# Optimization experiments

Hardware: AMD Instinct MI355X
Metric: run time of the kernel (lower is better)

Reference implementation:

```python
import jax, jax.numpy as jnp
import numpy as np

B, N, C = 2, 100000, 256
H, D, S = 8, 64, 64
INNER = H * D

def setup_inputs() -> dict:
    key = jax.random.key(0)
    ks = jax.random.split(key, 5)
    x = jax.random.normal(ks[0], (B, N, C), dtype=jnp.float32)
    W_x = jax.random.normal(ks[1], (C, INNER), dtype=jnp.float32) / np.sqrt(C)
    b_x = jnp.zeros((INNER,), dtype=jnp.float32)
    W_fx = jax.random.normal(ks[2], (C, INNER), dtype=jnp.float32) / np.sqrt(C)
    b_fx = jnp.zeros((INNER,), dtype=jnp.float32)
    W_slice = jax.random.normal(ks[3], (D, S), dtype=jnp.float32) / np.sqrt(D)
    b_slice = jnp.zeros((S,), dtype=jnp.float32)
    temperature = jnp.ones((1, 1, H, 1), dtype=jnp.float32) * 0.5
    return {"x": x, "W_x": W_x, "b_x": b_x, "W_fx": W_fx, "b_fx": b_fx,
            "W_slice": W_slice, "b_slice": b_slice, "temperature": temperature}

def reference(x, W_x, b_x, W_fx, b_fx, W_slice, b_slice, temperature):
    b, n, _ = x.shape
    # linear projections to (B, N, H, D)
    px = (x @ W_x + b_x).reshape(b, n, H, D)   # query-like projection
    fx = (x @ W_fx + b_fx).reshape(b, n, H, D) # feature (value) projection
    # slice logits (B, N, H, S)
    slice_proj = jnp.einsum('bnhd,ds->bnhs', px, W_slice) + b_slice
    temp = jnp.clip(temperature, 0.1, 5.0)     # (1,1,H,1), broadcast over S
    slice_weights = jax.nn.softmax(slice_proj / temp, axis=-1)  # (B,N,H,S)
    slice_norm = slice_weights.sum(axis=1)     # (B,H,S)
    # weighted aggregation of tokens into slice tokens (B,H,S,D)
    slice_token = jnp.einsum('bnhs,bnhd->bhsd', slice_weights, fx)
    slice_token = slice_token / (slice_norm[..., None] + 1e-5)
    return slice_token
```

## Files before the change

kernel.cpp:

```cpp
#include <hip/hip_runtime.h>
#include <hip/hip_bf16.h>
#include <cstdint>

#define B_     2
#define N_     100000
#define C_     256
#define H_     8
#define D_     64
#define S_     64
#define INNER_ 512

#define TILE_T 64
#define NTILES ((N_ + TILE_T - 1) / TILE_T)
#define PBLK   32

#define WEFFT_OFF 0
#define WFXT_OFF  262144
#define BIASE_OFF 524288
#define SLAB_OFF  526336
#define NSLAB_OFF (SLAB_OFF + B_*H_*PBLK*4096*4)
#define WS_BIG_END (NSLAB_OFF + B_*H_*PBLK*64*4)
#define ACC_OFF   526336
#define NRM_OFF   (ACC_OFF + B_*H_*S_*D_*4)
#define WS_SMALL_END (NRM_OFF + B_*H_*S_*4)

typedef __attribute__((ext_vector_type(8))) short short8;
typedef __attribute__((ext_vector_type(4))) float f32x4;

__device__ inline short f2bf(float f) {
    __hip_bfloat16 h = __float2bfloat16(f);
    short s; __builtin_memcpy(&s, &h, 2); return s;
}
__device__ inline uint32_t pk2(float a, float b) {
    __hip_bfloat162 h = __float22bfloat162_rn(float2{a, b});
    uint32_t u; __builtin_memcpy(&u, &h, 4); return u;
}

__global__ void prep_kernel(const float* __restrict__ W_x,
                            const float* __restrict__ b_x,
                            const float* __restrict__ W_fx,
                            const float* __restrict__ W_slice,
                            const float* __restrict__ b_slice,
                            const float* __restrict__ temperature,
                            uint8_t* __restrict__ wsb) {
    int wid  = (blockIdx.x * 256 + threadIdx.x) >> 6;
    int lane = threadIdx.x & 63;
    if (wid < H_ * C_) {
        int h = wid >> 8, k = wid & 255;
        float t = temperature[h]; t = fminf(fmaxf(t, 0.1f), 5.0f);
        float sc = 1.44269504088896f / t;
        const float* wx = W_x + k * INNER_ + h * 64;
        float a = 0.f;
        #pragma unroll 8
        for (int d = 0; d < D_; ++d)
            a = fmaf(wx[d], W_slice[d * 64 + lane], a);
        ((short*)(wsb + WEFFT_OFF))[(h * 64 + lane) * 256 + k] = f2bf(a * sc);
    } else if (wid < 2 * H_ * C_) {
        int j = wid - H_ * C_;
        int h = j >> 8, k = j & 255;
        ((short*)(wsb + WFXT_OFF))[(h * 64 + lane) * 256 + k] =
            f2bf(W_fx[k * INNER_ + h * 64 + lane]);
    } else if (wid < 2 * H_ * C_ + H_) {
        int h = wid - 2 * H_ * C_;
        float t = temperature[h]; t = fminf(fmaxf(t, 0.1f), 5.0f);
        float sc = 1.44269504088896f / t;
        float a = 0.f;
        #pragma unroll 8
        for (int d = 0; d < D_; ++d)
            a = fmaf(b_x[h * 64 + d], W_slice[d * 64 + lane], a);
        ((float*)(wsb + BIASE_OFF))[h * 64 + lane] = (a + b_slice[lane]) * sc;
    }
}

template<bool SLAB>
__global__ __launch_bounds__(512, 4) void main_kernel(
        const float* __restrict__ x,
        const float* __restrict__ b_fx,
        const uint8_t* __restrict__ wsb,
        float* __restrict__ accg,
        float* __restrict__ nrmg) {
    __shared__ union {
        short xs[TILE_T * 264];
        struct { short wsl[S_ * 72]; short fsl[D_ * 72]; } wf;
    } u;
    __shared__ float smB[TILE_T * 4];

    const int tid = threadIdx.x;
    const int bid = blockIdx.x;
    const int cc = bid & 7;
    const int h  = (bid >> 3) & 7;
    const int pb = (bid >> 6) * 8 + cc;
    const int p  = pb & 31;
    const int b  = pb >> 5;

    const int lane = tid & 63, wv = tid >> 6;
    const int l = lane & 15, q = lane >> 4;
    const int g  = wv >> 2;
    const int w4 = wv & 3;

    const short* wT = (const short*)(wsb + (g ? WFXT_OFF : WEFFT_OFF)) + h * (64 * 256);
    short8 breg[8];
    #pragma unroll
    for (int k = 0; k < 8; ++k)
        breg[k] = *(const short8*)(wT + (w4 * 16 + l) * 256 + k * 32 + q * 8);

    const float bias_n = g ? b_fx[h * 64 + w4 * 16 + l]
                           : ((const float*)(wsb + BIASE_OFF))[h * 64 + w4 * 16 + l];

    const float* xb = x + (size_t)b * ((size_t)N_ * C_);
    f32x4 accO[2] = {};
    float nrmacc = 0.f;

    float4 xv[8];
    {
        const int col = lane * 4;
        #pragma unroll
        for (int j = 0; j < 8; ++j) {
            int gt = p * TILE_T + wv + 8 * j;
            xv[j] = (gt < N_) ? *(const float4*)(xb + (size_t)gt * C_ + col)
                              : float4{0.f, 0.f, 0.f, 0.f};
        }
    }

    #pragma unroll 1
    for (int tile = p; tile < NTILES; tile += PBLK) {
        __syncthreads();
        {
            #pragma unroll
            for (int j = 0; j < 8; ++j) {
                int row = wv + 8 * j;
                uint2 pk = { pk2(xv[j].x, xv[j].y), pk2(xv[j].z, xv[j].w) };
                *(uint2*)(u.xs + row * 264 + lane * 4) = pk;
            }
        }
        __syncthreads();

        {
            int nxt = tile + PBLK;
            if (nxt < NTILES) {
                const int col = lane * 4;
                #pragma unroll
                for (int j = 0; j < 8; ++j) {
                    int gt = nxt * TILE_T + wv + 8 * j;
                    xv[j] = (gt < N_) ? *(const float4*)(xb + (size_t)gt * C_ + col)
                                      : float4{0.f, 0.f, 0.f, 0.f};
                }
            }
        }

        f32x4 acc[4] = {};
        #pragma unroll
        for (int k = 0; k < 8; ++k) {
            #pragma unroll
            for (int m = 0; m < 4; ++m) {
                short8 a = *(const short8*)(u.xs + (m * 16 + l) * 264 + k * 32 + q * 8);
                acc[m] = __builtin_amdgcn_mfma_f32_16x16x32_bf16(a, breg[k], acc[m], 0, 0, 0);
            }
        }

        if (g == 0) {
            #pragma unroll
            for (int m = 0; m < 4; ++m)
                #pragma unroll
                for (int r = 0; r < 4; ++r) {
                    float e = __builtin_amdgcn_exp2f(acc[m][r] + bias_n);
                    acc[m][r] = e;
                    float sv = e;
                    sv += __shfl_xor(sv, 1, 64);
                    sv += __shfl_xor(sv, 2, 64);
                    sv += __shfl_xor(sv, 4, 64);
                    sv += __shfl_xor(sv, 8, 64);
                    if (l == 0) smB[(m * 16 + q * 4 + r) * 4 + wv] = sv;
                }
        } else {
            #pragma unroll
            for (int m = 0; m < 4; ++m)
                #pragma unroll
                for (int r = 0; r < 4; ++r)
                    acc[m][r] += bias_n;
        }
        __syncthreads();

        const int t0 = tile * TILE_T;
        if (g == 0) {
            #pragma unroll
            for (int m = 0; m < 4; ++m) {
                #pragma unroll
                for (int r = 0; r < 4; ++r) {
                    int tok = m * 16 + q * 4 + r;
                    float4 s4 = *(const float4*)(smB + tok * 4);
                    float S = (s4.x + s4.y) + (s4.z + s4.w);
                    float f = __builtin_amdgcn_rcpf(S);
                    if (t0 + tok >= N_) f = 0.f;
                    float w = acc[m][r] * f;
                    acc[m][r] = w;
                    nrmacc += w;
                }
                uint2 pk = { pk2(acc[m][0], acc[m][1]), pk2(acc[m][2], acc[m][3]) };
                *(uint2*)(u.wf.wsl + (w4 * 16 + l) * 72 + m * 16 + q * 4) = pk;
            }
        } else {
            #pragma unroll
            for (int m = 0; m < 4; ++m) {
                uint2 pk = { pk2(acc[m][0], acc[m][1]), pk2(acc[m][2], acc[m][3]) };
                *(uint2*)(u.wf.fsl + (w4 * 16 + l) * 72 + m * 16 + q * 4) = pk;
            }
        }
        __syncthreads();

        #pragma unroll
        for (int kk = 0; kk < 2; ++kk) {
            short8 aw = *(const short8*)(u.wf.wsl + (w4 * 16 + l) * 72 + kk * 32 + q * 8);
            #pragma unroll
            for (int nt = 0; nt < 2; ++nt) {
                short8 bf = *(const short8*)(u.wf.fsl + (g * 32 + nt * 16 + l) * 72 + kk * 32 + q * 8);
                accO[nt] = __builtin_amdgcn_mfma_f32_16x16x32_bf16(aw, bf, accO[nt], 0, 0, 0);
            }
        }
    }

    if (SLAB) {
        float* sp = accg + ((size_t)(b * H_ + h) * PBLK + p) * 4096;
        #pragma unroll
        for (int nt = 0; nt < 2; ++nt)
            #pragma unroll
            for (int r = 0; r < 4; ++r)
                sp[(w4 * 16 + q * 4 + r) * 64 + g * 32 + nt * 16 + l] = accO[nt][r];
        if (g == 0) {
            float v = nrmacc;
            v += __shfl_xor(v, 16, 64);
            v += __shfl_xor(v, 32, 64);
            if (lane < 16)
                nrmg[((b * H_ + h) * PBLK + p) * 64 + w4 * 16 + lane] = v;
        }
    } else {
        float* ag = accg + (size_t)((b * H_ + h) * 64) * 64;
        #pragma unroll
        for (int nt = 0; nt < 2; ++nt)
            #pragma unroll
            for (int r = 0; r < 4; ++r)
                atomicAdd(ag + (w4 * 16 + q * 4 + r) * 64 + g * 32 + nt * 16 + l, accO[nt][r]);
        if (g == 0) {
            float v = nrmacc;
            v += __shfl_xor(v, 16, 64);
            v += __shfl_xor(v, 32, 64);
            if (lane < 16)
                atomicAdd(nrmg + (b * H_ + h) * 64 + w4 * 16 + lane, v);
        }
    }
}

__global__ void finalize_big(const float* __restrict__ slab,
                             const float* __restrict__ nslab,
                             float* __restrict__ out) {
    int idx = blockIdx.x * 256 + threadIdx.x;
    int bh = idx >> 12, sd = idx & 4095, s = sd >> 6;
    const float* sp = slab  + (size_t)bh * PBLK * 4096 + sd;
    const float* np = nslab + bh * PBLK * 64 + s;
    float acc = 0.f, nn = 0.f;
    #pragma unroll 8
    for (int p = 0; p < PBLK; ++p) { acc += sp[p * 4096]; nn += np[p * 64]; }
    out[idx] = acc / (nn + 1e-5f);
}

__global__ void finalize_small(const uint8_t* __restrict__ wsb, float* __restrict__ out) {
    int idx = blockIdx.x * 256 + threadIdx.x;
    float a = ((const float*)(wsb + ACC_OFF))[idx];
    float n = ((const float*)(wsb + NRM_OFF))[idx / D_];
    out[idx] = a / (n + 1e-5f);
}

extern "C" void kernel_launch(void* const* d_in, const int* in_sizes, int n_in,
                              void* d_out, int out_size, void* d_ws, size_t ws_size,
                              hipStream_t stream) {
    const float* x           = (const float*)d_in[0];
    const float* W_x         = (const float*)d_in[1];
    const float* b_x         = (const float*)d_in[2];
    const float* W_fx        = (const float*)d_in[3];
    const float* b_fx        = (const float*)d_in[4];
    const float* W_slice     = (const float*)d_in[5];
    const float* b_slice     = (const float*)d_in[6];
    const float* temperature = (const float*)d_in[7];
    float* out = (float*)d_out;
    uint8_t* wsb = (uint8_t*)d_ws;

    int prep_waves = 2 * H_ * C_ + H_;
    prep_kernel<<<dim3((prep_waves + 3) / 4), dim3(256), 0, stream>>>(
        W_x, b_x, W_fx, W_slice, b_slice, temperature, wsb);

    if (ws_size >= (size_t)WS_BIG_END) {
        main_kernel<true><<<dim3(PBLK * H_ * B_), dim3(512), 0, stream>>>(
            x, b_fx, wsb, (float*)(wsb + SLAB_OFF), (float*)(wsb + NSLAB_OFF));
        finalize_big<<<dim3(256), dim3(256), 0, stream>>>(
            (const float*)(wsb + SLAB_OFF), (const float*)(wsb + NSLAB_OFF), out);
    } else {
        hipMemsetAsync(wsb + ACC_OFF, 0, (B_ * H_ * S_ * D_ + B_ * H_ * S_) * 4, stream);
        main_kernel<false><<<dim3(PBLK * H_ * B_), dim3(512), 0, stream>>>(
            x, b_fx, wsb, (float*)(wsb + ACC_OFF), (float*)(wsb + NRM_OFF));
        finalize_small<<<dim3(256), dim3(256), 0, stream>>>(wsb, out);
    }
}
```

Measured before the change: 577.3 us.

## Re-tile projection MFMA as 2x2 per wave and split x prefetch

Each wave now computes a 32-token by 32-column block (2x2 MFMA tiles) instead of 64 tokens by 16 columns. This halves the shared-memory A-fragment loads per MFMA and changes the softmax row-sum reduction from 4 partials to 2. The LDS union is dropped so the x tile and the weight/feature tiles no longer alias, which removes one barrier per tile. The x row pitch is padded to 272. Half of each tile's x rows are now loaded directly inside the loop rather than prefetched, which cuts register use but exposes some global-load latency. It also doubles the B-fragment registers.

```diff
diff --git a/kernel.cpp b/kernel.cpp
--- a/kernel.cpp
+++ b/kernel.cpp
@@ -23,6 +23,8 @@
 #define ACC_OFF   526336
 #define NRM_OFF   (ACC_OFF + B_*H_*S_*D_*4)
 #define WS_SMALL_END (NRM_OFF + B_*H_*S_*4)
+
+#define XSP 272
 
 typedef __attribute__((ext_vector_type(8))) short short8;
 typedef __attribute__((ext_vector_type(4))) float f32x4;
@@ -79,11 +81,10 @@
         const uint8_t* __restrict__ wsb,
         float* __restrict__ accg,
         float* __restrict__ nrmg) {
-    __shared__ union {
-        short xs[TILE_T * 264];
-        struct { short wsl[S_ * 72]; short fsl[D_ * 72]; } wf;
-    } u;
-    __shared__ float smB[TILE_T * 4];
+    __shared__ short xs[TILE_T * XSP];
+    __shared__ short wsl[S_ * 72];
+    __shared__ short fsl[D_ * 72];
+    __shared__ float smB[TILE_T * 2];
 
     const int tid = threadIdx.x;
     const int bid = blockIdx.x;
@@ -95,27 +96,34 @@
 
     const int lane = tid & 63, wv = tid >> 6;
     const int l = lane & 15, q = lane >> 4;
-    const int g  = wv >> 2;
-    const int w4 = wv & 3;
+    const int g  = wv & 1;
+    const int nh = (wv >> 1) & 1;
+    const int th = wv >> 2;
 
     const short* wT = (const short*)(wsb + (g ? WFXT_OFF : WEFFT_OFF)) + h * (64 * 256);
-    short8 breg[8];
+    short8 breg[2][8];
     #pragma unroll
-    for (int k = 0; k < 8; ++k)
-        breg[k] = *(const short8*)(wT + (w4 * 16 + l) * 256 + k * 32 + q * 8);
-
-    const float bias_n = g ? b_fx[h * 64 + w4 * 16 + l]
-                           : ((const float*)(wsb + BIASE_OFF))[h * 64 + w4 * 16 + l];
+    for (int nt = 0; nt < 2; ++nt)
+        #pragma unroll
+        for (int k = 0; k < 8; ++k)
+            breg[nt][k] = *(const short8*)(wT + (nh * 32 + nt * 16 + l) * 256 + k * 32 + q * 8);
+
+    float bias_n[2];
+    #pragma unroll
+    for (int nt = 0; nt < 2; ++nt) {
+        int n = nh * 32 + nt * 16 + l;
+        bias_n[nt] = g ? b_fx[h * 64 + n] : ((const float*)(wsb + BIASE_OFF))[h * 64 + n];
+    }
 
     const float* xb = x + (size_t)b * ((size_t)N_ * C_);
     f32x4 accO[2] = {};
-    float nrmacc = 0.f;
-
-    float4 xv[8];
+    float nrmacc[2] = {0.f, 0.f};
+
+    float4 xv[4];
     {
         const int col = lane * 4;
         #pragma unroll
-        for (int j = 0; j < 8; ++j) {
+        for (int j = 0; j < 4; ++j) {
             int gt = p * TILE_T + wv + 8 * j;
             xv[j] = (gt < N_) ? *(const float4*)(xb + (size_t)gt * C_ + col)
                               : float4{0.f, 0.f, 0.f, 0.f};
@@ -124,13 +132,27 @@
 
     #pragma unroll 1
     for (int tile = p; tile < NTILES; tile += PBLK) {
-        __syncthreads();
+        const int t0 = tile * TILE_T;
         {
-            #pragma unroll
-            for (int j = 0; j < 8; ++j) {
+            const int col = lane * 4;
+            float4 dv4[4];
+            #pragma unroll
+            for (int j = 0; j < 4; ++j) {
+                int gt = t0 + wv + 8 * (j + 4);
+                dv4[j] = (gt < N_) ? *(const float4*)(xb + (size_t)gt * C_ + col)
+                                   : float4{0.f, 0.f, 0.f, 0.f};
+            }
+            #pragma unroll
+            for (int j = 0; j < 4; ++j) {
                 int row = wv + 8 * j;
                 uint2 pk = { pk2(xv[j].x, xv[j].y), pk2(xv[j].z, xv[j].w) };
-                *(uint2*)(u.xs + row * 264 + lane * 4) = pk;
+                *(uint2*)(xs + row * XSP + col) = pk;
+            }
+            #pragma unroll
+            for (int j = 0; j < 4; ++j) {
+                int row = wv + 8 * (j + 4);
+                uint2 pk = { pk2(dv4[j].x, dv4[j].y), pk2(dv4[j].z, dv4[j].w) };
+                *(uint2*)(xs + row * XSP + col) = pk;
             }
         }
         __syncthreads();
@@ -140,7 +162,7 @@
             if (nxt < NTILES) {
                 const int col = lane * 4;
                 #pragma unroll
-                for (int j = 0; j < 8; ++j) {
+                for (int j = 0; j < 4; ++j) {
                     int gt = nxt * TILE_T + wv + 8 * j;
                     xv[j] = (gt < N_) ? *(const float4*)(xb + (size_t)gt * C_ + col)
                                       : float4{0.f, 0.f, 0.f, 0.f};
@@ -148,104 +170,126 @@
             }
         }
 
-        f32x4 acc[4] = {};
+        f32x4 acc[2][2] = {};
         #pragma unroll
         for (int k = 0; k < 8; ++k) {
-            #pragma unroll
-            for (int m = 0; m < 4; ++m) {
-                short8 a = *(const short8*)(u.xs + (m * 16 + l) * 264 + k * 32 + q * 8);
-                acc[m] = __builtin_amdgcn_mfma_f32_16x16x32_bf16(a, breg[k], acc[m], 0, 0, 0);
+            short8 a0 = *(const short8*)(xs + (th * 32 + l) * XSP + k * 32 + q * 8);
+            short8 a1 = *(const short8*)(xs + (th * 32 + 16 + l) * XSP + k * 32 + q * 8);
+            #pragma unroll
+            for (int nt = 0; nt < 2; ++nt) {
+                acc[0][nt] = __builtin_amdgcn_mfma_f32_16x16x32_bf16(a0, breg[nt][k], acc[0][nt], 0, 0, 0);
+                acc[1][nt] = __builtin_amdgcn_mfma_f32_16x16x32_bf16(a1, breg[nt][k], acc[1][nt], 0, 0, 0);
             }
         }
 
         if (g == 0) {
             #pragma unroll
-            for (int m = 0; m < 4; ++m)
+            for (int m = 0; m < 2; ++m)
                 #pragma unroll
                 for (int r = 0; r < 4; ++r) {
-                    float e = __builtin_amdgcn_exp2f(acc[m][r] + bias_n);
-                    acc[m][r] = e;
-                    float sv = e;
+                    float e0 = __builtin_amdgcn_exp2f(acc[m][0][r] + bias_n[0]);
+                    float e1 = __builtin_amdgcn_exp2f(acc[m][1][r] + bias_n[1]);
+                    acc[m][0][r] = e0; acc[m][1][r] = e1;
+                    float sv = e0 + e1;
                     sv += __shfl_xor(sv, 1, 64);
                     sv += __shfl_xor(sv, 2, 64);
                     sv += __shfl_xor(sv, 4, 64);
                     sv += __shfl_xor(sv, 8, 64);
-                    if (l == 0) smB[(m * 16 + q * 4 + r) * 4 + wv] = sv;
+                    if (l == 0)
+                        smB[(th * 32 + m * 16 + q * 4 + r) * 2 + nh] = sv;
                 }
         } else {
             #pragma unroll
-            for (int m = 0; m < 4; ++m)
-                #pragma unroll
-                for (int r = 0; r < 4; ++r)
-                    acc[m][r] += bias_n;
+            for (int m = 0; m < 2; ++m)
+                #pragma unroll
+                for (int nt = 0; nt < 2; ++nt) {
+                    int dd = nh * 32 + nt * 16 + l, tt = th * 32 + m * 16 + q * 4;
+                    uint2 pk = { pk2(acc[m][nt][0] + bias_n[nt], acc[m][nt][1] + bias_n[nt]),
+                                 pk2(acc[m][nt][2] + bias_n[nt], acc[m][nt][3] + bias_n[nt]) };
+                    *(uint2*)(fsl + dd * 72 + tt) = pk;
+                }
         }
         __syncthreads();
 
-        const int t0 = tile * TILE_T;
         if (g == 0) {
             #pragma unroll
-            for (int m = 0; m < 4; ++m) {
+            for (int m = 0; m < 2; ++m) {
                 #pragma unroll
                 for (int r = 0; r < 4; ++r) {
-                    int tok = m * 16 + q * 4 + r;
-                    float4 s4 = *(const float4*)(smB + tok * 4);
-                    float S = (s4.x + s4.y) + (s4.z + s4.w);
+                    int tok = th * 32 + m * 16 + q * 4 + r;
+                    float2 s2 = *(const float2*)(smB + tok * 2);
+                    float S = s2.x + s2.y;
                     float f = __builtin_amdgcn_rcpf(S);
                     if (t0 + tok >= N_) f = 0.f;
-                    float w = acc[m][r] * f;
-                    acc[m][r] = w;
-                    nrmacc += w;
-                }
-                uint2 pk = { pk2(acc[m][0], acc[m][1]), pk2(acc[m][2], acc[m][3]) };
-                *(uint2*)(u.wf.wsl + (w4 * 16 + l) * 72 + m * 16 + q * 4) = pk;
-            }
+                    float w0 = acc[m][0][r] * f, w1 = acc[m][1][r] * f;
+                    nrmacc[0] += w0; nrmacc[1] += w1;
+                    acc[m][0][r] = w0; acc[m][1][r] = w1;
+                }
+                #pragma unroll
+                for (int nt = 0; nt < 2; ++nt) {
+                    int ss = nh * 32 + nt * 16 + l, tt = th * 32 + m * 16 + q * 4;
+                    uint2 pk = { pk2(acc[m][nt][0], acc[m][nt][1]),
+                                 pk2(acc[m][nt][2], acc[m][nt][3]) };
+                    *(uint2*)(wsl + ss * 72 + tt) = pk;
+                }
+            }
+        }
+        __syncthreads();
+
+        {
+            const int sv_ = wv & 3, dv = wv >> 2;
+            #pragma unroll
+            for (int kk = 0; kk < 2; ++kk) {
+                short8 aw = *(const short8*)(wsl + (sv_ * 16 + l) * 72 + kk * 32 + q * 8);
+                #pragma unroll
+                for (int nt = 0; nt < 2; ++nt) {
+                    short8 bf = *(const short8*)(fsl + (dv * 32 + nt * 16 + l) * 72 + kk * 32 + q * 8);
+                    accO[nt] = __builtin_amdgcn_mfma_f32_16x16x32_bf16(aw, bf, accO[nt], 0, 0, 0);
+                }
+            }
+        }
+    }
+
+    {
+        const int sv_ = wv & 3, dv = wv >> 2;
+        if (SLAB) {
+            float* sp = accg + ((size_t)(b * H_ + h) * PBLK + p) * 4096;
+            #pragma unroll
+            for (int nt = 0; nt < 2; ++nt)
+                #pragma unroll
+                for (int r = 0; r < 4; ++r)
+                    sp[(sv_ * 16 + q * 4 + r) * 64 + dv * 32 + nt * 16 + l] = accO[nt][r];
         } else {
-            #pragma unroll
-            for (int m = 0; m < 4; ++m) {
-                uint2 pk = { pk2(acc[m][0], acc[m][1]), pk2(acc[m][2], acc[m][3]) };
-                *(uint2*)(u.wf.fsl + (w4 * 16 + l) * 72 + m * 16 + q * 4) = pk;
-            }
-        }
-        __syncthreads();
-
-        #pragma unroll
-        for (int kk = 0; kk < 2; ++kk) {
-            short8 aw = *(const short8*)(u.wf.wsl + (w4 * 16 + l) * 72 + kk * 32 + q * 8);
-            #pragma unroll
-            for (int nt = 0; nt < 2; ++nt) {
-                short8 bf = *(const short8*)(u.wf.fsl + (g * 32 + nt * 16 + l) * 72 + kk * 32 + q * 8);
-                accO[nt] = __builtin_amdgcn_mfma_f32_16x16x32_bf16(aw, bf, accO[nt], 0, 0, 0);
-            }
-        }
-    }
-
-    if (SLAB) {
-        float* sp = accg + ((size_t)(b * H_ + h) * PBLK + p) * 4096;
-        #pragma unroll
-        for (int nt = 0; nt < 2; ++nt)
-            #pragma unroll
-            for (int r = 0; r < 4; ++r)
-                sp[(w4 * 16 + q * 4 + r) * 64 + g * 32 + nt * 16 + l] = accO[nt][r];
-        if (g == 0) {
-            float v = nrmacc;
+            float* ag = accg + (size_t)((b * H_ + h) * 64) * 64;
+            #pragma unroll
+            for (int nt = 0; nt < 2; ++nt)
+                #pragma unroll
+                for (int r = 0; r < 4; ++r)
+                    atomicAdd(ag + (sv_ * 16 + q * 4 + r) * 64 + dv * 32 + nt * 16 + l, accO[nt][r]);
+        }
+    }
+
+    __syncthreads();
+    if (g == 0) {
+        #pragma unroll
+        for (int nt = 0; nt < 2; ++nt) {
+            float v = nrmacc[nt];
             v += __shfl_xor(v, 16, 64);
             v += __shfl_xor(v, 32, 64);
             if (lane < 16)
-                nrmg[((b * H_ + h) * PBLK + p) * 64 + w4 * 16 + lane] = v;
-        }
-    } else {
-        float* ag = accg + (size_t)((b * H_ + h) * 64) * 64;
-        #pragma unroll
-        for (int nt = 0; nt < 2; ++nt)
-            #pragma unroll
-            for (int r = 0; r < 4; ++r)
-                atomicAdd(ag + (w4 * 16 + q * 4 + r) * 64 + g * 32 + nt * 16 + l, accO[nt][r]);
-        if (g == 0) {
-            float v = nrmacc;
-            v += __shfl_xor(v, 16, 64);
-            v += __shfl_xor(v, 32, 64);
-            if (lane < 16)
-                atomicAdd(nrmg + (b * H_ + h) * 64 + w4 * 16 + lane, v);
+                smB[(nh * 32 + nt * 16 + lane) * 2 + th] = v;
+        }
+    }
+    __syncthreads();
+    if (g == 0 && th == 0 && lane < 16) {
+        #pragma unroll
+        for (int nt = 0; nt < 2; ++nt) {
+            int s = nh * 32 + nt * 16 + lane;
+            float v = smB[s * 2] + smB[s * 2 + 1];
+            if (SLAB)
+                nrmg[((b * H_ + h) * PBLK + p) * 64 + s] = v;
+            else
+                atomicAdd(nrmg + (b * H_ + h) * 64 + s, v);
         }
     }
 }
```

Result: slower. 679.0 us (+17.6%).
